# Kernel tuning notes

Hardware: AMD Instinct MI355X
Metric: run time of the kernel (lower is better)

The kernel has to match this reference:

```python
import jax, jax.numpy as jnp
import numpy as np

EMB = 1024
HEADS = 16
BLOCK = 128


def setup_inputs() -> dict:
    key = jax.random.key(0)
    k1, k2, k3 = jax.random.split(key, 3)
    B, T, C = 4, 4096, EMB
    x = jax.random.normal(k1, (B, T, C), dtype=jnp.float32)
    # Linear weights stored as [in, out] (i.e. torch W.T); qkv has no bias.
    W_qkv = jax.random.normal(k2, (C, 3 * C), dtype=jnp.float32) * 0.02
    W_proj = jax.random.normal(k3, (C, C), dtype=jnp.float32) * 0.02
    b_proj = jnp.zeros((C,), dtype=jnp.float32)
    return {"x": x, "W_qkv": W_qkv, "W_proj": W_proj, "b_proj": b_proj}


def reference(x, W_qkv, W_proj, b_proj):
    # Dropout is inference-mode identity.
    B, T, C = x.shape
    H, D, BS = HEADS, C // HEADS, BLOCK
    nb = T // BS  # number of local blocks
    qkv = x @ W_qkv  # [B,T,3C]
    q, k, v = jnp.split(qkv, 3, axis=-1)
    # [B, nb, BS, H, D] -- each block attends only within itself
    q = q.reshape(B, nb, BS, H, D)
    k = k.reshape(B, nb, BS, H, D)
    v = v.reshape(B, nb, BS, H, D)
    scores = jnp.einsum("bnqhd,bnkhd->bnhqk", q, k) / jnp.sqrt(jnp.float32(D))
    # is_decoder: causal tril within each diagonal block (tril[i:end, i:end])
    tril = jnp.tril(jnp.ones((BS, BS), dtype=bool))
    scores = jnp.where(tril, scores, -jnp.inf)
    # faithful to original: stable exp, then divide by (sum + 1e-6)
    scores = scores - jnp.max(scores, axis=-1, keepdims=True)
    e = jnp.exp(scores)
    p = e / (jnp.sum(e, axis=-1, keepdims=True) + 1e-6)
    out = jnp.einsum("bnhqk,bnkhd->bnqhd", p, v).reshape(B, T, C)
    return out @ W_proj + b_proj
```

## Files before the change

kernel.cpp:

```cpp
#include <hip/hip_runtime.h>
#include <hip/hip_bf16.h>
#include <math.h>


typedef __bf16 bf16_t;
typedef __bf16 bf16x8 __attribute__((ext_vector_type(8)));
typedef float  f32x4  __attribute__((ext_vector_type(4)));

typedef const __attribute__((address_space(1))) void* gptr_t;
typedef __attribute__((address_space(3))) void* lptr_t;

__global__ __launch_bounds__(256) void cvt_f32_bf16(const float* __restrict__ in,
                                                    bf16_t* __restrict__ out, size_t n) {
    size_t stride = (size_t)gridDim.x * blockDim.x * 4;
    for (size_t i = ((size_t)blockIdx.x * blockDim.x + threadIdx.x) * 4; i < n; i += stride) {
        float4 v = *(const float4*)(in + i);
        bf16_t t[4];
        t[0] = (bf16_t)v.x; t[1] = (bf16_t)v.y; t[2] = (bf16_t)v.z; t[3] = (bf16_t)v.w;
        *(uint2*)(out + i) = *(uint2*)t;
    }
}

__global__ __launch_bounds__(256) void transpose_cvt(const float* __restrict__ in,
                                                     bf16_t* __restrict__ out, int K, int N) {
    __shared__ float tile[32][33];
    const int tx = threadIdx.x & 31, ty = threadIdx.x >> 5;
    const int bx = blockIdx.x, by = blockIdx.y;
    #pragma unroll
    for (int i = 0; i < 4; i++) {
        const int k = by * 32 + ty + i * 8;
        tile[ty + i * 8][tx] = in[(size_t)k * N + bx * 32 + tx];
    }
    __syncthreads();
    #pragma unroll
    for (int i = 0; i < 4; i++) {
        const int n = bx * 32 + ty + i * 8;
        out[(size_t)n * K + by * 32 + tx] = (bf16_t)tile[tx][ty + i * 8];
    }
}

template <bool BF16_OUT, bool BIAS>
__global__ __launch_bounds__(512, 2) void gemm256(const bf16_t* __restrict__ A,
                                                  const bf16_t* __restrict__ Bt,
                                                  void* __restrict__ Cout,
                                                  const float* __restrict__ bias,
                                                  int M, int N, int K) {
    __shared__ bf16_t As[4][256 * 32];
    __shared__ bf16_t Bs[4][256 * 32];

    const int tid  = threadIdx.x;
    const int lane = tid & 63, wave = tid >> 6;
    const int quad = lane >> 4, l16 = lane & 15;
    const int wm = wave >> 2, wn = wave & 3;
    const int bn = blockIdx.x, bm = blockIdx.y;

    const bf16_t* Ab = A  + (size_t)bm * 256 * K;
    const bf16_t* Bb = Bt + (size_t)bn * 256 * K;

    const int srow = lane >> 2;
    const int scs  = (lane & 3) ^ ((srow >> 1) & 3);
    const int csw  = (l16 >> 1) & 3;

    f32x4 acc[8][4];
    #pragma unroll
    for (int i = 0; i < 8; ++i)
        #pragma unroll
        for (int j = 0; j < 4; ++j) acc[i][j] = (f32x4){0.f, 0.f, 0.f, 0.f};

#define STG(ARR, SRC, SLOT, SLICE, I)                                                 \
    __builtin_amdgcn_global_load_lds(                                                 \
        (gptr_t)((SRC) + (size_t)(wave * 32 + (I) * 16 + srow) * K + (SLICE) * 32 +   \
                 scs * 8),                                                            \
        (lptr_t)&(ARR)[SLOT][(wave * 32 + (I) * 16) * 32], 16, 0, 0)

#define STAGE4(SLICE)                                                                 \
    do {                                                                              \
        const int sl_ = (SLICE) & 3;                                                  \
        STG(As, Ab, sl_, SLICE, 0); STG(As, Ab, sl_, SLICE, 1);                       \
        STG(Bs, Bb, sl_, SLICE, 0); STG(Bs, Bb, sl_, SLICE, 1);                       \
    } while (0)

#define COMPUTE(KS)                                                                   \
    do {                                                                              \
        const bf16_t* Asl_ = As[(KS) & 3];                                            \
        const bf16_t* Bsl_ = Bs[(KS) & 3];                                            \
        bf16x8 af_[8], bf_[4];                                                        \
        _Pragma("unroll")                                                             \
        for (int fr = 0; fr < 8; ++fr)                                                \
            af_[fr] = *(const bf16x8*)&Asl_[(wm * 128 + fr * 16 + l16) * 32 +         \
                                            ((quad ^ csw) << 3)];                     \
        _Pragma("unroll")                                                             \
        for (int fr = 0; fr < 4; ++fr)                                                \
            bf_[fr] = *(const bf16x8*)&Bsl_[(wn * 64 + fr * 16 + l16) * 32 +          \
                                            ((quad ^ csw) << 3)];                     \
        __builtin_amdgcn_s_setprio(1);                                                \
        _Pragma("unroll")                                                             \
        for (int mr = 0; mr < 8; ++mr)                                                \
            _Pragma("unroll")                                                         \
            for (int nr = 0; nr < 4; ++nr)                                            \
                acc[mr][nr] = __builtin_amdgcn_mfma_f32_16x16x32_bf16(                \
                    af_[mr], bf_[nr], acc[mr][nr], 0, 0, 0);                          \
        __builtin_amdgcn_s_setprio(0);                                                \
    } while (0)

    #pragma unroll
    for (int s = 0; s < 3; ++s) STAGE4(s);

    const int NS = K >> 5;
    for (int ks = 0; ks < NS - 3; ++ks) {
        asm volatile("s_waitcnt vmcnt(8)" ::: "memory");
        __builtin_amdgcn_s_barrier();
        STAGE4(ks + 3);
        COMPUTE(ks);
    }
    {
        asm volatile("s_waitcnt vmcnt(8)" ::: "memory");
        __builtin_amdgcn_s_barrier();
        COMPUTE(NS - 3);
        asm volatile("s_waitcnt vmcnt(4)" ::: "memory");
        __builtin_amdgcn_s_barrier();
        COMPUTE(NS - 2);
        asm volatile("s_waitcnt vmcnt(0)" ::: "memory");
        __builtin_amdgcn_s_barrier();
        COMPUTE(NS - 1);
    }
#undef COMPUTE
#undef STAGE4
#undef STG

    #pragma unroll
    for (int mr = 0; mr < 8; ++mr) {
        #pragma unroll
        for (int nr = 0; nr < 4; ++nr) {
            const int gcol = bn * 256 + wn * 64 + nr * 16 + l16;
            #pragma unroll
            for (int reg = 0; reg < 4; ++reg) {
                const int grow = bm * 256 + wm * 128 + mr * 16 + quad * 4 + reg;
                float v = acc[mr][nr][reg];
                if (BIAS) v += bias[gcol];
                if (BF16_OUT)
                    ((bf16_t*)Cout)[(size_t)grow * N + gcol] = (bf16_t)v;
                else
                    ((float*)Cout)[(size_t)grow * N + gcol] = v;
            }
        }
    }
}

__global__ __launch_bounds__(256, 3) void attn_kernel(const bf16_t* __restrict__ qkv,
                                                      bf16_t* __restrict__ attn_out) {
    __shared__ __align__(16) char smem[54272];
    bf16_t* qs = (bf16_t*)smem;
    bf16_t* ks = (bf16_t*)(smem + 18432);
    bf16_t* vT = (bf16_t*)(smem + 36864);
    bf16_t* ps = (bf16_t*)smem;

    const int tid = threadIdx.x;
    const int lane = tid & 63, wave = tid >> 6;
    const int quad = lane >> 4, l16 = lane & 15;

    const int bid = blockIdx.x;
    const int h = bid & 15;
    const int blk = (bid >> 4) & 31;
    const int b = bid >> 9;
    const int row0 = (b * 32 + blk) * 128;
    const int LDQ = 3072;

    for (int t = tid; t < 128 * 8; t += 256) {
        const int r = t >> 3;
        const int c = (t & 7) * 8;
        const bf16_t* src = qkv + (size_t)(row0 + r) * LDQ + h * 64;
        *(uint4*)&qs[r * 72 + c] = *(const uint4*)(src + c);
        *(uint4*)&ks[r * 72 + c] = *(const uint4*)(src + 1024 + c);
        bf16x8 vv = *(const bf16x8*)(src + 2048 + c);
        #pragma unroll
        for (int j = 0; j < 8; j++)
            vT[(c + j) * 136 + r] = vv[j];
    }
    __syncthreads();

    f32x4 sfrag[2][8];
    for (int mr = 0; mr < 2; mr++)
        for (int nc = 0; nc < 8; nc++)
            sfrag[mr][nc] = (f32x4){0.f, 0.f, 0.f, 0.f};

    #pragma unroll
    for (int ksl = 0; ksl < 2; ksl++) {
        bf16x8 aq[2], bk[8];
        #pragma unroll
        for (int mr = 0; mr < 2; mr++)
            aq[mr] = *(const bf16x8*)&qs[(wave * 32 + mr * 16 + l16) * 72 + ksl * 32 + quad * 8];
        #pragma unroll
        for (int nc = 0; nc < 8; nc++)
            bk[nc] = *(const bf16x8*)&ks[(nc * 16 + l16) * 72 + ksl * 32 + quad * 8];
        #pragma unroll
        for (int mr = 0; mr < 2; mr++)
            #pragma unroll
            for (int nc = 0; nc < 8; nc++)
                sfrag[mr][nc] = __builtin_amdgcn_mfma_f32_16x16x32_bf16(aq[mr], bk[nc], sfrag[mr][nc], 0, 0, 0);
    }

    #pragma unroll
    for (int mr = 0; mr < 2; mr++) {
        #pragma unroll
        for (int nc = 0; nc < 8; nc++) {
            #pragma unroll
            for (int reg = 0; reg < 4; reg++) {
                const int row = wave * 32 + mr * 16 + quad * 4 + reg;
                const int col = nc * 16 + l16;
                float s = sfrag[mr][nc][reg] * 0.125f;
                if (col > row) s = -INFINITY;
                sfrag[mr][nc][reg] = s;
            }
        }
    }

    #pragma unroll
    for (int mr = 0; mr < 2; mr++) {
        #pragma unroll
        for (int reg = 0; reg < 4; reg++) {
            float m = -INFINITY;
            #pragma unroll
            for (int nc = 0; nc < 8; nc++) m = fmaxf(m, sfrag[mr][nc][reg]);
            #pragma unroll
            for (int off = 1; off < 16; off <<= 1) m = fmaxf(m, __shfl_xor(m, off));
            float sum = 0.f;
            #pragma unroll
            for (int nc = 0; nc < 8; nc++) {
                float e = __expf(sfrag[mr][nc][reg] - m);
                sfrag[mr][nc][reg] = e;
                sum += e;
            }
            #pragma unroll
            for (int off = 1; off < 16; off <<= 1) sum += __shfl_xor(sum, off);
            const float inv = 1.0f / (sum + 1e-6f);
            #pragma unroll
            for (int nc = 0; nc < 8; nc++) sfrag[mr][nc][reg] *= inv;
        }
    }

    __syncthreads();

    #pragma unroll
    for (int mr = 0; mr < 2; mr++)
        #pragma unroll
        for (int nc = 0; nc < 8; nc++)
            #pragma unroll
            for (int reg = 0; reg < 4; reg++) {
                const int row = wave * 32 + mr * 16 + quad * 4 + reg;
                const int col = nc * 16 + l16;
                ps[row * 136 + col] = (bf16_t)sfrag[mr][nc][reg];
            }
    __syncthreads();

    f32x4 oacc[2][4];
    for (int mr = 0; mr < 2; mr++)
        for (int nd = 0; nd < 4; nd++)
            oacc[mr][nd] = (f32x4){0.f, 0.f, 0.f, 0.f};

    #pragma unroll
    for (int ksl = 0; ksl < 4; ksl++) {
        bf16x8 ap[2];
        #pragma unroll
        for (int mr = 0; mr < 2; mr++)
            ap[mr] = *(const bf16x8*)&ps[(wave * 32 + mr * 16 + l16) * 136 + ksl * 32 + quad * 8];
        #pragma unroll
        for (int nd = 0; nd < 4; nd++) {
            bf16x8 bv = *(const bf16x8*)&vT[(nd * 16 + l16) * 136 + ksl * 32 + quad * 8];
            #pragma unroll
            for (int mr = 0; mr < 2; mr++)
                oacc[mr][nd] = __builtin_amdgcn_mfma_f32_16x16x32_bf16(ap[mr], bv, oacc[mr][nd], 0, 0, 0);
        }
    }

    #pragma unroll
    for (int mr = 0; mr < 2; mr++)
        #pragma unroll
        for (int nd = 0; nd < 4; nd++)
            #pragma unroll
            for (int reg = 0; reg < 4; reg++) {
                const int row = row0 + wave * 32 + mr * 16 + quad * 4 + reg;
                const int col = h * 64 + nd * 16 + l16;
                attn_out[(size_t)row * 1024 + col] = (bf16_t)oacc[mr][nd][reg];
            }
}

extern "C" void kernel_launch(void* const* d_in, const int* in_sizes, int n_in,
                              void* d_out, int out_size, void* d_ws, size_t ws_size,
                              hipStream_t stream) {
    const float* x     = (const float*)d_in[0];
    const float* Wqkv  = (const float*)d_in[1];
    const float* Wproj = (const float*)d_in[2];
    const float* bproj = (const float*)d_in[3];

    const int M = 16384, C = 1024, N1 = 3072;

    char* ws = (char*)d_ws;
    bf16_t* xb     = (bf16_t*)(ws);
    bf16_t* wqkvT  = (bf16_t*)(ws + 33554432);
    bf16_t* wprojT = (bf16_t*)(ws + 39845888);
    bf16_t* qkvb   = (bf16_t*)(ws + 41943040);
    bf16_t* attnb  = (bf16_t*)(ws + 142606336);

    cvt_f32_bf16<<<8192, 256, 0, stream>>>(x, xb, (size_t)M * C);
    transpose_cvt<<<dim3(N1 / 32, C / 32), 256, 0, stream>>>(Wqkv, wqkvT, C, N1);
    transpose_cvt<<<dim3(C / 32, C / 32), 256, 0, stream>>>(Wproj, wprojT, C, C);

    gemm256<true, false><<<dim3(N1 / 256, M / 256), 512, 0, stream>>>(
        xb, wqkvT, (void*)qkvb, nullptr, M, N1, C);

    attn_kernel<<<2048, 256, 0, stream>>>(qkvb, attnb);

    gemm256<false, true><<<dim3(C / 256, M / 256), 512, 0, stream>>>(
        attnb, wprojT, d_out, bproj, M, C, C);
}
```

Before: 347.4 us.

## Split GEMM k-slice into two ping-pong halves interleaving loads with MFMA

Restructures the GEMM main loop so each k-slice runs as two halves. Each half issues part of the LDS fragment reads and part of the global-to-LDS staging, then runs 16 MFMAs, separated by extra barriers. This is an 8-wave ping-pong style schedule meant to overlap memory traffic with matrix-core work and to ease register pressure by loading A fragments in two steps. In exchange it adds four barriers per slice, and the changed vmcnt accounting risks stalls or ordering hazards.

```diff
diff --git a/kernel.cpp b/kernel.cpp
--- a/kernel.cpp
+++ b/kernel.cpp
@@ -59,7 +59,7 @@
 
     const int srow = lane >> 2;
     const int scs  = (lane & 3) ^ ((srow >> 1) & 3);
-    const int csw  = (l16 >> 1) & 3;
+    const int rdo  = ((quad ^ ((l16 >> 1) & 3)) << 3);
 
     f32x4 acc[8][4];
     #pragma unroll
@@ -67,65 +67,70 @@
         #pragma unroll
         for (int j = 0; j < 4; ++j) acc[i][j] = (f32x4){0.f, 0.f, 0.f, 0.f};
 
-#define STG(ARR, SRC, SLOT, SLICE, I)                                                 \
+#define STG(ARR, SRC, SLICE, I)                                                       \
     __builtin_amdgcn_global_load_lds(                                                 \
-        (gptr_t)((SRC) + (size_t)(wave * 32 + (I) * 16 + srow) * K + (SLICE) * 32 +   \
+        (gptr_t)((SRC) + (size_t)(wave * 32 + (I) * 16 + srow) * K + ((SLICE) << 5) + \
                  scs * 8),                                                            \
-        (lptr_t)&(ARR)[SLOT][(wave * 32 + (I) * 16) * 32], 16, 0, 0)
-
-#define STAGE4(SLICE)                                                                 \
+        (lptr_t)&(ARR)[(SLICE) & 3][(wave * 32 + (I) * 16) * 32], 16, 0, 0)
+
+#define SLICE_BODY(KS, DO_STAGE, WAIT_STMT)                                           \
     do {                                                                              \
-        const int sl_ = (SLICE) & 3;                                                  \
-        STG(As, Ab, sl_, SLICE, 0); STG(As, Ab, sl_, SLICE, 1);                       \
-        STG(Bs, Bb, sl_, SLICE, 0); STG(Bs, Bb, sl_, SLICE, 1);                       \
-    } while (0)
-
-#define COMPUTE(KS)                                                                   \
-    do {                                                                              \
-        const bf16_t* Asl_ = As[(KS) & 3];                                            \
-        const bf16_t* Bsl_ = Bs[(KS) & 3];                                            \
+        const int ks_ = (KS);                                                         \
+        const bf16_t* Asl_ = As[ks_ & 3];                                             \
+        const bf16_t* Bsl_ = Bs[ks_ & 3];                                             \
         bf16x8 af_[8], bf_[4];                                                        \
-        _Pragma("unroll")                                                             \
-        for (int fr = 0; fr < 8; ++fr)                                                \
-            af_[fr] = *(const bf16x8*)&Asl_[(wm * 128 + fr * 16 + l16) * 32 +         \
-                                            ((quad ^ csw) << 3)];                     \
+                             \
         _Pragma("unroll")                                                             \
         for (int fr = 0; fr < 4; ++fr)                                                \
-            bf_[fr] = *(const bf16x8*)&Bsl_[(wn * 64 + fr * 16 + l16) * 32 +          \
-                                            ((quad ^ csw) << 3)];                     \
+            af_[fr] = *(const bf16x8*)&Asl_[(wm * 128 + fr * 16 + l16) * 32 + rdo];   \
+        _Pragma("unroll")                                                             \
+        for (int fr = 0; fr < 4; ++fr)                                                \
+            bf_[fr] = *(const bf16x8*)&Bsl_[(wn * 64 + fr * 16 + l16) * 32 + rdo];    \
+        if (DO_STAGE) { STG(As, Ab, ks_ + 3, 0); STG(As, Ab, ks_ + 3, 1); }           \
+        __builtin_amdgcn_s_barrier();                                                 \
+        asm volatile("s_waitcnt lgkmcnt(0)" ::: "memory");                            \
         __builtin_amdgcn_s_setprio(1);                                                \
         _Pragma("unroll")                                                             \
-        for (int mr = 0; mr < 8; ++mr)                                                \
+        for (int mr = 0; mr < 4; ++mr)                                                \
             _Pragma("unroll")                                                         \
             for (int nr = 0; nr < 4; ++nr)                                            \
                 acc[mr][nr] = __builtin_amdgcn_mfma_f32_16x16x32_bf16(                \
                     af_[mr], bf_[nr], acc[mr][nr], 0, 0, 0);                          \
         __builtin_amdgcn_s_setprio(0);                                                \
+        __builtin_amdgcn_s_barrier();                                                 \
+              \
+        _Pragma("unroll")                                                             \
+        for (int fr = 0; fr < 4; ++fr)                                                \
+            af_[4 + fr] =                                                             \
+                *(const bf16x8*)&Asl_[(wm * 128 + (4 + fr) * 16 + l16) * 32 + rdo];   \
+        if (DO_STAGE) { STG(Bs, Bb, ks_ + 3, 0); STG(Bs, Bb, ks_ + 3, 1); }           \
+        WAIT_STMT;                                                                    \
+        __builtin_amdgcn_s_barrier();                                                 \
+        asm volatile("s_waitcnt lgkmcnt(0)" ::: "memory");                            \
+        __builtin_amdgcn_s_setprio(1);                                                \
+        _Pragma("unroll")                                                             \
+        for (int mr = 0; mr < 4; ++mr)                                                \
+            _Pragma("unroll")                                                         \
+            for (int nr = 0; nr < 4; ++nr)                                            \
+                acc[4 + mr][nr] = __builtin_amdgcn_mfma_f32_16x16x32_bf16(            \
+                    af_[4 + mr], bf_[nr], acc[4 + mr][nr], 0, 0, 0);                  \
+        __builtin_amdgcn_s_setprio(0);                                                \
+        __builtin_amdgcn_s_barrier();                                                 \
     } while (0)
 
-    #pragma unroll
-    for (int s = 0; s < 3; ++s) STAGE4(s);
+    STG(As, Ab, 0, 0); STG(As, Ab, 0, 1); STG(Bs, Bb, 0, 0); STG(Bs, Bb, 0, 1);
+    STG(As, Ab, 1, 0); STG(As, Ab, 1, 1); STG(Bs, Bb, 1, 0); STG(Bs, Bb, 1, 1);
+    STG(As, Ab, 2, 0); STG(As, Ab, 2, 1); STG(Bs, Bb, 2, 0); STG(Bs, Bb, 2, 1);
+    asm volatile("s_waitcnt vmcnt(8)" ::: "memory");
+    __builtin_amdgcn_s_barrier();
 
     const int NS = K >> 5;
-    for (int ks = 0; ks < NS - 3; ++ks) {
-        asm volatile("s_waitcnt vmcnt(8)" ::: "memory");
-        __builtin_amdgcn_s_barrier();
-        STAGE4(ks + 3);
-        COMPUTE(ks);
-    }
-    {
-        asm volatile("s_waitcnt vmcnt(8)" ::: "memory");
-        __builtin_amdgcn_s_barrier();
-        COMPUTE(NS - 3);
-        asm volatile("s_waitcnt vmcnt(4)" ::: "memory");
-        __builtin_amdgcn_s_barrier();
-        COMPUTE(NS - 2);
-        asm volatile("s_waitcnt vmcnt(0)" ::: "memory");
-        __builtin_amdgcn_s_barrier();
-        COMPUTE(NS - 1);
-    }
-#undef COMPUTE
-#undef STAGE4
+    for (int ks = 0; ks < NS - 3; ++ks)
+        SLICE_BODY(ks, true, asm volatile("s_waitcnt vmcnt(8)" ::: "memory"));
+    SLICE_BODY(NS - 3, false, asm volatile("s_waitcnt vmcnt(4)" ::: "memory"));
+    SLICE_BODY(NS - 2, false, asm volatile("s_waitcnt vmcnt(0)" ::: "memory"));
+    SLICE_BODY(NS - 1, false, (void)0);
+#undef SLICE_BODY
 #undef STG
 
     #pragma unroll
```

After: 321.7 us. 7.4% less time.
